# Performance work log

Measured on AMD Instinct MI355X. Metric: run time of the kernel, lower is better.

## Reference

```python
import jax, jax.numpy as jnp
import numpy as np

N_NODES = 50000


def _add_self_loops(edge_index, n):
    loop = jnp.arange(n, dtype=edge_index.dtype)
    src = jnp.concatenate([edge_index[0], loop])
    dst = jnp.concatenate([edge_index[1], loop])
    return src, dst


def _gcn_norm(src, dst, n):
    # symmetric normalization with unit edge weights (edge_weight=None)
    w = jnp.ones(src.shape[0], dtype=jnp.float32)
    deg = jax.ops.segment_sum(w, dst, num_segments=n)  # [N]
    dinv = jnp.where(deg > 0, jax.lax.rsqrt(jnp.maximum(deg, 1.0)), 0.0)
    return dinv[src] * w * dinv[dst]  # [E+N]


def _gcn_conv(x, src, dst, norm, W, b, n):
    h = x @ W                                   # [N, out] transform first (PyG order)
    msg = h[src] * norm[:, None]                # [E+N, out] gather + scale
    agg = jax.ops.segment_sum(msg, dst, num_segments=n)  # scatter-add
    return agg + b


def setup_inputs() -> dict:
    key = jax.random.key(0)
    k1, k2, k3, k4 = jax.random.split(key, 4)
    N, E, IN, HID, OUT = N_NODES, 1600000, 512, 64, 7
    x = jax.random.normal(k1, (N, IN), dtype=jnp.float32)
    edge_index = jax.random.randint(k2, (2, E), 0, N, dtype=jnp.int64)
    W1 = jax.random.normal(k3, (IN, HID), dtype=jnp.float32) * (1.0 / np.sqrt(IN))
    b1 = jnp.zeros((HID,), dtype=jnp.float32)
    W2 = jax.random.normal(k4, (HID, OUT), dtype=jnp.float32) * (1.0 / np.sqrt(HID))
    b2 = jnp.zeros((OUT,), dtype=jnp.float32)
    return {"x": x, "edge_index": edge_index, "W1": W1, "b1": b1, "W2": W2, "b2": b2}


def reference(x, edge_index, W1, b1, W2, b2):
    n = x.shape[0]
    src, dst = _add_self_loops(edge_index, n)
    norm = _gcn_norm(src, dst, n)  # graph-only, shared across layers
    h = _gcn_conv(x, src, dst, norm, W1, b1, n)
    h = jax.nn.relu(h)
    # dropout is identity in eval/inference mode
    out = _gcn_conv(h, src, dst, norm, W2, b2, n)
    return out
```

## Files before the change

### kernel.cpp

```cpp
#include <hip/hip_runtime.h>

#define N_NODES 50000
#define N_EDGES 1600000
#define DIM_IN  512
#define DIM_HID 64
#define DIM_OUT 7
#define NBUCK   196
#define PART_BLOCKS 256

using u16 = unsigned short;
using bf16x8 = __attribute__((ext_vector_type(8))) __bf16;
using f32x4  = __attribute__((ext_vector_type(4))) float;

__device__ __forceinline__ float bf2f(u16 u) {
    union { float f; unsigned int i; } v;
    v.i = ((unsigned int)u) << 16;
    return v.f;
}

__device__ __forceinline__ u16 f2bf(float f) {
    union { float f; unsigned int i; } v;
    v.f = f;
    unsigned int r = 0x7FFFu + ((v.i >> 16) & 1u);
    return (u16)((v.i + r) >> 16);
}

__device__ __forceinline__ float bflo(unsigned int u) {
    union { float f; unsigned int i; } v;
    v.i = u << 16;
    return v.f;
}

__device__ __forceinline__ float bfhi(unsigned int u) {
    union { float f; unsigned int i; } v;
    v.i = u & 0xFFFF0000u;
    return v.f;
}

__global__ void k_detect(const u16* __restrict__ xw, const int* __restrict__ ei32,
                         int* __restrict__ flags) {
    __shared__ int s1[256];
    __shared__ int s2[256];
    int t = threadIdx.x;
    u16 w = xw[2 * t];
    int e = (w >> 7) & 0xFF;
    s1[t] = (e >= 100 && e <= 140) ? 1 : 0;
    s2[t] = (ei32[2 * t + 1] != 0) ? 1 : 0;
    __syncthreads();
    for (int off = 128; off >= 1; off >>= 1) {
        if (t < off) { s1[t] += s1[t + off]; s2[t] += s2[t + off]; }
        __syncthreads();
    }
    if (t == 0) {
        flags[0] = (s1[0] >= 200) ? 0 : 1;
        flags[1] = (s2[0] == 0) ? 1 : 0;
    }
}

__device__ __forceinline__ int ld_edge(const int* ei, int i64f, size_t idx) {
    if (i64f) return ei[2 * idx];
    return ei[idx];
}

__global__ void k_count(const int* __restrict__ ei, const int* __restrict__ flags,
                        int* __restrict__ gbsum, int* __restrict__ cnt) {
    __shared__ int hist[NBUCK];
    int t = threadIdx.x;
    int i64f = flags[1];
    const int CH = (N_EDGES + PART_BLOCKS - 1) / PART_BLOCKS;
    int lo = blockIdx.x * CH;
    int hi = lo + CH; if (hi > N_EDGES) hi = N_EDGES;
    if (t < NBUCK) hist[t] = 0;
    __syncthreads();
    for (int i = lo + t; i < hi; i += 1024) {
        int s = ld_edge(ei, i64f, (size_t)i);
        int d = ld_edge(ei, i64f, (size_t)N_EDGES + i);
        if ((unsigned)d < (unsigned)N_NODES && (unsigned)s < (unsigned)N_NODES)
            atomicAdd(&hist[d >> 8], 1);
    }
    __syncthreads();
    if (t < NBUCK) {
        int h = hist[t];
        cnt[t * PART_BLOCKS + blockIdx.x] = h;
        if (h > 0) atomicAdd(&gbsum[t], h);
    }
}

__global__ void k_pb(const int* __restrict__ gbsum, int* __restrict__ cnt,
                     int* __restrict__ bbase, int* __restrict__ rowptr) {
    __shared__ int g0[256];
    __shared__ int gs[256];
    __shared__ int sc[256];
    int b = blockIdx.x, t = threadIdx.x;
    int gv = (t < NBUCK) ? gbsum[t] : 0;
    g0[t] = gv;
    gs[t] = gv;
    __syncthreads();
    for (int off = 1; off < 256; off <<= 1) {
        int u = (t >= off) ? gs[t - off] : 0;
        __syncthreads();
        gs[t] += u;
        __syncthreads();
    }
    int bb = gs[b] - g0[b];
    if (t == 0) bbase[b] = bb;
    if (b == 0 && t == 255) rowptr[N_NODES] = gs[255];
    int v = cnt[b * PART_BLOCKS + t];
    sc[t] = v;
    __syncthreads();
    for (int off = 1; off < 256; off <<= 1) {
        int u = (t >= off) ? sc[t - off] : 0;
        __syncthreads();
        sc[t] += u;
        __syncthreads();
    }
    cnt[b * PART_BLOCKS + t] = bb + sc[t] - v;
}

__global__ void k_part(const int* __restrict__ ei, const int* __restrict__ flags,
                       const int* __restrict__ cnt, unsigned int* __restrict__ ebuf) {
    __shared__ int cur[NBUCK];
    int t = threadIdx.x, blk = blockIdx.x;
    int i64f = flags[1];
    const int CH = (N_EDGES + PART_BLOCKS - 1) / PART_BLOCKS;
    int lo = blk * CH;
    int hi = lo + CH; if (hi > N_EDGES) hi = N_EDGES;
    if (t < NBUCK) cur[t] = cnt[t * PART_BLOCKS + blk];
    __syncthreads();
    for (int i = lo + t; i < hi; i += 1024) {
        int s = ld_edge(ei, i64f, (size_t)i);
        int d = ld_edge(ei, i64f, (size_t)N_EDGES + i);
        if ((unsigned)d < (unsigned)N_NODES && (unsigned)s < (unsigned)N_NODES) {
            int pos = atomicAdd(&cur[d >> 8], 1);
            if ((unsigned)pos < (unsigned)N_EDGES)
                ebuf[pos] = ((unsigned)s << 8) | (unsigned)(d & 255);
        }
    }
}

__global__ void k_cfill(const unsigned int* __restrict__ ebuf,
                        const int* __restrict__ bbase, const int* __restrict__ gbsum,
                        int* __restrict__ rowptr, float* __restrict__ dinv,
                        int* __restrict__ col) {
    __shared__ int dcnt[256];
    __shared__ int sc[256];
    __shared__ int cur[256];
    int b = blockIdx.x, t = threadIdx.x;
    int e0 = bbase[b];
    int e1 = e0 + gbsum[b];
    if (t < 256) dcnt[t] = 0;
    __syncthreads();
    for (int e = e0 + t; e < e1; e += 1024)
        atomicAdd(&dcnt[ebuf[e] & 255u], 1);
    __syncthreads();
    int v = 0;
    if (t < 256) { v = dcnt[t]; sc[t] = v; }
    __syncthreads();
    for (int off = 1; off < 256; off <<= 1) {
        int u = (t >= off && t < 256) ? sc[t - off] : 0;
        __syncthreads();
        if (t < 256) sc[t] += u;
        __syncthreads();
    }
    if (t < 256) {
        int row0 = e0 + sc[t] - v;
        cur[t] = row0;
        int idx = b * 256 + t;
        if (idx < N_NODES) {
            rowptr[idx] = row0;
            dinv[idx] = rsqrtf((float)(v + 1));
        }
    }
    __syncthreads();
    for (int e = e0 + t; e < e1; e += 1024) {
        unsigned int x = ebuf[e];
        int p = atomicAdd(&cur[x & 255u], 1);
        if ((unsigned)p < (unsigned)N_EDGES) col[p] = (int)(x >> 8);
    }
}

__global__ void k_tw1(const void* __restrict__ W1, const int* __restrict__ flags,
                      u16* __restrict__ W1T) {
    int i = blockIdx.x * blockDim.x + threadIdx.x;
    if (i < DIM_IN * DIM_HID) {
        int n = i >> 9;
        int k = i & 511;
        if (flags[0]) W1T[i] = f2bf(((const float*)W1)[k * DIM_HID + n]);
        else          W1T[i] = ((const u16*)W1)[k * DIM_HID + n];
    }
}

__launch_bounds__(256)
__global__ void k_gemm1(const void* __restrict__ xraw, const u16* __restrict__ W1T,
                        const int* __restrict__ flags, const float* __restrict__ dinv,
                        u16* __restrict__ hs) {
    int f32f = flags[0];
    int wave = threadIdx.x >> 6;
    int lane = threadIdx.x & 63;
    int m16 = lane & 15;
    int quad = lane >> 4;
    int rbase = blockIdx.x * 64 + wave * 16;
    int ra = rbase + m16;
    if (ra > N_NODES - 1) ra = N_NODES - 1;
    const u16*   xrow_b = (const u16*)xraw   + (size_t)ra * DIM_IN + quad * 8;
    const float* xrow_f = (const float*)xraw + (size_t)ra * DIM_IN + quad * 8;
    const u16* wrow = W1T + (size_t)m16 * DIM_IN + quad * 8;

    f32x4 acc0 = {0.f, 0.f, 0.f, 0.f};
    f32x4 acc1 = {0.f, 0.f, 0.f, 0.f};
    f32x4 acc2 = {0.f, 0.f, 0.f, 0.f};
    f32x4 acc3 = {0.f, 0.f, 0.f, 0.f};

    for (int ks = 0; ks < DIM_IN / 32; ++ks) {
        bf16x8 a;
        if (f32f) {
            const float4* q = reinterpret_cast<const float4*>(xrow_f + ks * 32);
            float4 p0 = q[0], p1 = q[1];
            union { bf16x8 v; u16 s[8]; } u;
            u.s[0] = f2bf(p0.x); u.s[1] = f2bf(p0.y); u.s[2] = f2bf(p0.z); u.s[3] = f2bf(p0.w);
            u.s[4] = f2bf(p1.x); u.s[5] = f2bf(p1.y); u.s[6] = f2bf(p1.z); u.s[7] = f2bf(p1.w);
            a = u.v;
        } else {
            a = *reinterpret_cast<const bf16x8*>(xrow_b + ks * 32);
        }
        bf16x8 b0 = *reinterpret_cast<const bf16x8*>(wrow + ks * 32);
        bf16x8 b1 = *reinterpret_cast<const bf16x8*>(wrow + ks * 32 + 16 * DIM_IN);
        bf16x8 b2 = *reinterpret_cast<const bf16x8*>(wrow + ks * 32 + 32 * DIM_IN);
        bf16x8 b3 = *reinterpret_cast<const bf16x8*>(wrow + ks * 32 + 48 * DIM_IN);
        acc0 = __builtin_amdgcn_mfma_f32_16x16x32_bf16(a, b0, acc0, 0, 0, 0);
        acc1 = __builtin_amdgcn_mfma_f32_16x16x32_bf16(a, b1, acc1, 0, 0, 0);
        acc2 = __builtin_amdgcn_mfma_f32_16x16x32_bf16(a, b2, acc2, 0, 0, 0);
        acc3 = __builtin_amdgcn_mfma_f32_16x16x32_bf16(a, b3, acc3, 0, 0, 0);
    }

#pragma unroll
    for (int i = 0; i < 4; ++i) {
        int r = rbase + quad * 4 + i;
        if (r < N_NODES) {
            float dv = dinv[r];
            u16* orow = hs + (size_t)r * DIM_HID;
            orow[ 0 + m16] = f2bf(acc0[i] * dv);
            orow[16 + m16] = f2bf(acc1[i] * dv);
            orow[32 + m16] = f2bf(acc2[i] * dv);
            orow[48 + m16] = f2bf(acc3[i] * dv);
        }
    }
}

__launch_bounds__(256)
__global__ void k_agg1(const u16* __restrict__ hs, const int* __restrict__ rowptr,
                       const int* __restrict__ col, const float* __restrict__ dinv,
                       const void* __restrict__ b1, const void* __restrict__ W2,
                       const int* __restrict__ flags, float* __restrict__ zs) {
    __shared__ float xh[4][64];
    int f32f = flags[0];
    int wave = threadIdx.x >> 6;
    int lane = threadIdx.x & 63;
    int g = lane >> 3;
    int q = lane & 7;
    int d = blockIdx.x * 4 + wave;
    int start = rowptr[d], end = rowptr[d + 1];
    if (start < 0) start = 0;
    if (end > N_EDGES) end = N_EDGES;
    if (end < start) end = start;

    float a[8];
#pragma unroll
    for (int k = 0; k < 8; ++k) a[k] = 0.f;

    const uint4* hs4 = reinterpret_cast<const uint4*>(hs);
    const int* cp = col + start;
    int ne = end - start;
    int nfull = ne >> 3;

    int it = 0;
    for (; it + 4 <= nfull; it += 4) {
        int c0 = cp[(it + 0) * 8 + g];
        int c1 = cp[(it + 1) * 8 + g];
        int c2 = cp[(it + 2) * 8 + g];
        int c3 = cp[(it + 3) * 8 + g];
        uint4 r0 = hs4[(size_t)c0 * 8 + q];
        uint4 r1 = hs4[(size_t)c1 * 8 + q];
        uint4 r2 = hs4[(size_t)c2 * 8 + q];
        uint4 r3 = hs4[(size_t)c3 * 8 + q];
#pragma unroll
        for (int u = 0; u < 4; ++u) {
            uint4 r = (u == 0) ? r0 : (u == 1) ? r1 : (u == 2) ? r2 : r3;
            a[0] += bflo(r.x); a[1] += bfhi(r.x);
            a[2] += bflo(r.y); a[3] += bfhi(r.y);
            a[4] += bflo(r.z); a[5] += bfhi(r.z);
            a[6] += bflo(r.w); a[7] += bfhi(r.w);
        }
    }
    for (; it < nfull; ++it) {
        int c = cp[it * 8 + g];
        uint4 r = hs4[(size_t)c * 8 + q];
        a[0] += bflo(r.x); a[1] += bfhi(r.x);
        a[2] += bflo(r.y); a[3] += bfhi(r.y);
        a[4] += bflo(r.z); a[5] += bfhi(r.z);
        a[6] += bflo(r.w); a[7] += bfhi(r.w);
    }
    {
        int e = start + nfull * 8 + g;
        if (e < end) {
            int c = col[e];
            uint4 r = hs4[(size_t)c * 8 + q];
            a[0] += bflo(r.x); a[1] += bfhi(r.x);
            a[2] += bflo(r.y); a[3] += bfhi(r.y);
            a[4] += bflo(r.z); a[5] += bfhi(r.z);
            a[6] += bflo(r.w); a[7] += bfhi(r.w);
        }
    }

#pragma unroll
    for (int k = 0; k < 8; ++k) {
        a[k] += __shfl_xor(a[k], 8);
        a[k] += __shfl_xor(a[k], 16);
        a[k] += __shfl_xor(a[k], 32);
    }

    {
        uint4 r = hs4[(size_t)d * 8 + q];
        a[0] += bflo(r.x); a[1] += bfhi(r.x);
        a[2] += bflo(r.y); a[3] += bfhi(r.y);
        a[4] += bflo(r.z); a[5] += bfhi(r.z);
        a[6] += bflo(r.w); a[7] += bfhi(r.w);
    }

    float dv = dinv[d];
    float h[8];
    if (f32f) {
        const float* bf = (const float*)b1 + q * 8;
#pragma unroll
        for (int k = 0; k < 8; ++k) h[k] = fmaxf(a[k] * dv + bf[k], 0.f);
    } else {
        const u16* bb = (const u16*)b1 + q * 8;
#pragma unroll
        for (int k = 0; k < 8; ++k) h[k] = fmaxf(a[k] * dv + bf2f(bb[k]), 0.f);
    }

    if (g == 0) {
#pragma unroll
        for (int k = 0; k < 8; ++k) xh[wave][q * 8 + k] = h[k];
    }
    __syncthreads();
    float h2 = xh[wave][lane];

    float p[7];
#pragma unroll
    for (int f = 0; f < 7; ++f) {
        float w = f32f ? ((const float*)W2)[lane * DIM_OUT + f]
                       : bf2f(((const u16*)W2)[lane * DIM_OUT + f]);
        p[f] = h2 * w;
    }
#pragma unroll
    for (int off = 32; off >= 1; off >>= 1) {
#pragma unroll
        for (int f = 0; f < 7; ++f) p[f] += __shfl_xor(p[f], off);
    }
    if (lane == 0) {
#pragma unroll
        for (int f = 0; f < 7; ++f) zs[(size_t)d * 8 + f] = p[f] * dv;
        zs[(size_t)d * 8 + 7] = 0.f;
    }
}

__launch_bounds__(256)
__global__ void k_agg2(const float* __restrict__ zs, const int* __restrict__ rowptr,
                       const int* __restrict__ col, const float* __restrict__ dinv,
                       const void* __restrict__ b2, const int* __restrict__ flags,
                       float* __restrict__ out) {
    int f32f = flags[0];
    int wave = threadIdx.x >> 6;
    int lane = threadIdx.x & 63;
    int d = blockIdx.x * 4 + wave;
    if (d >= N_NODES) return;
    int f = lane & 7;
    int g = lane >> 3;
    int start = rowptr[d], end = rowptr[d + 1];
    if (start < 0) start = 0;
    if (end > N_EDGES) end = N_EDGES;
    if (end < start) end = start;

    float acc = 0.f;
    for (int e = start + g; e < end; e += 8)
        acc += zs[(size_t)col[e] * 8 + f];

    acc += __shfl_xor(acc, 8);
    acc += __shfl_xor(acc, 16);
    acc += __shfl_xor(acc, 32);

    if (lane < 7) {
        float b2v = f32f ? ((const float*)b2)[lane] : bf2f(((const u16*)b2)[lane]);
        float tot = (acc + zs[(size_t)d * 8 + lane]) * dinv[d] + b2v;
        out[(size_t)d * DIM_OUT + lane] = tot;
    }
}

extern "C" void kernel_launch(void* const* d_in, const int* in_sizes, int n_in,
                              void* d_out, int out_size, void* d_ws, size_t ws_size,
                              hipStream_t stream) {
    const void* x  = d_in[0];
    const int*  ei = (const int*)d_in[1];
    const void* W1 = d_in[2];
    const void* b1 = d_in[3];
    const void* W2 = d_in[4];
    const void* b2 = d_in[5];

    char* ws = (char*)d_ws;
    size_t off = 0;
    auto alloc = [&](size_t bytes) -> void* {
        void* p = ws + off;
        off = (off + bytes + 255) & ~(size_t)255;
        return p;
    };
    int*   flags  = (int*)alloc(32);
    int*   rowptr = (int*)alloc((size_t)(N_NODES + 1) * 4);
    int*   gbsum  = (int*)alloc((size_t)NBUCK * 4);
    int*   bbase  = (int*)alloc((size_t)NBUCK * 4);
    int*   cnt    = (int*)alloc((size_t)NBUCK * PART_BLOCKS * 4);
    float* dinv   = (float*)alloc((size_t)N_NODES * 4);
    u16*   W1T    = (u16*)alloc((size_t)DIM_IN * DIM_HID * 2);
    unsigned int* ebuf = (unsigned int*)alloc((size_t)N_EDGES * 4);
    int*   colb   = (int*)alloc((size_t)N_EDGES * 4);
    u16*   hs     = (u16*)alloc((size_t)N_NODES * DIM_HID * 2);
    float* zs     = (float*)alloc((size_t)N_NODES * 8 * 4);
    float* out    = (float*)d_out;

    hipMemsetAsync(gbsum, 0, (size_t)NBUCK * 4, stream);
    k_detect<<<1, 256, 0, stream>>>((const u16*)x, ei, flags);
    k_count<<<PART_BLOCKS, 1024, 0, stream>>>(ei, flags, gbsum, cnt);
    k_pb   <<<NBUCK, 256, 0, stream>>>(gbsum, cnt, bbase, rowptr);
    k_part <<<PART_BLOCKS, 1024, 0, stream>>>(ei, flags, cnt, ebuf);
    k_cfill<<<NBUCK, 1024, 0, stream>>>(ebuf, bbase, gbsum, rowptr, dinv, colb);
    k_tw1  <<<(DIM_IN * DIM_HID + 255) / 256, 256, 0, stream>>>(W1, flags, W1T);
    k_gemm1<<<(N_NODES + 63) / 64, 256, 0, stream>>>(x, W1T, flags, dinv, hs);
    k_agg1 <<<(N_NODES + 3) / 4, 256, 0, stream>>>(hs, rowptr, colb, dinv, b1, W2, flags, zs);
    k_agg2 <<<(N_NODES + 3) / 4, 256, 0, stream>>>(zs, rowptr, colb, dinv, b2, flags, out);
}
```

Measured before the change: 296.1 us.

## Fuse CSR build into fixed-capacity bucket scatter and merge prep kernels

Replaces the count / prefix-sum / partition kernel sequence with a single scatter kernel. Each block reserves space in a fixed-capacity per-bucket buffer through a global atomic, and the bucket prefix sum moves into the column-fill kernel. Detection, counter zeroing and the W1 transpose are merged into one single-block prep kernel, which removes the memset and several launches. The cost is a larger edge buffer and silent truncation of any bucket holding more than BCAP edges. It also makes the W1 transpose serial on one block and the intra-bucket edge order nondeterministic.

```diff
diff --git a/kernel.cpp b/kernel.cpp
--- a/kernel.cpp
+++ b/kernel.cpp
@@ -7,6 +7,7 @@
 #define DIM_OUT 7
 #define NBUCK   196
 #define PART_BLOCKS 256
+#define BCAP    16384
 
 using u16 = unsigned short;
 using bf16x8 = __attribute__((ext_vector_type(8))) __bf16;
@@ -37,121 +38,114 @@
     return v.f;
 }
 
-__global__ void k_detect(const u16* __restrict__ xw, const int* __restrict__ ei32,
-                         int* __restrict__ flags) {
+__device__ __forceinline__ int ld_edge(const int* ei, int i64f, size_t idx) {
+    if (i64f) return ei[2 * idx];
+    return ei[idx];
+}
+
+__launch_bounds__(1024)
+__global__ void k_prep(const u16* __restrict__ xw, const int* __restrict__ ei32,
+                       const void* __restrict__ W1, int* __restrict__ flags,
+                       int* __restrict__ gcnt, u16* __restrict__ W1T) {
     __shared__ int s1[256];
     __shared__ int s2[256];
+    __shared__ int fl0;
     int t = threadIdx.x;
-    u16 w = xw[2 * t];
-    int e = (w >> 7) & 0xFF;
-    s1[t] = (e >= 100 && e <= 140) ? 1 : 0;
-    s2[t] = (ei32[2 * t + 1] != 0) ? 1 : 0;
+    if (t < 256) {
+        u16 w = xw[2 * t];
+        int e = (w >> 7) & 0xFF;
+        s1[t] = (e >= 100 && e <= 140) ? 1 : 0;
+        s2[t] = (ei32[2 * t + 1] != 0) ? 1 : 0;
+    }
     __syncthreads();
     for (int off = 128; off >= 1; off >>= 1) {
         if (t < off) { s1[t] += s1[t + off]; s2[t] += s2[t + off]; }
         __syncthreads();
     }
     if (t == 0) {
-        flags[0] = (s1[0] >= 200) ? 0 : 1;
+        int f0 = (s1[0] >= 200) ? 0 : 1;
+        flags[0] = f0;
         flags[1] = (s2[0] == 0) ? 1 : 0;
-    }
-}
-
-__device__ __forceinline__ int ld_edge(const int* ei, int i64f, size_t idx) {
-    if (i64f) return ei[2 * idx];
-    return ei[idx];
-}
-
-__global__ void k_count(const int* __restrict__ ei, const int* __restrict__ flags,
-                        int* __restrict__ gbsum, int* __restrict__ cnt) {
+        fl0 = f0;
+    }
+    if (t < NBUCK) gcnt[t] = 0;
+    __syncthreads();
+    int f32f = fl0;
+    for (int i = t; i < DIM_IN * DIM_HID; i += 1024) {
+        int n = i >> 9;
+        int k = i & 511;
+        if (f32f) W1T[i] = f2bf(((const float*)W1)[k * DIM_HID + n]);
+        else      W1T[i] = ((const u16*)W1)[k * DIM_HID + n];
+    }
+}
+
+__launch_bounds__(1024)
+__global__ void k_scat(const int* __restrict__ ei, const int* __restrict__ flags,
+                       int* __restrict__ gcnt, unsigned int* __restrict__ ebuf) {
     __shared__ int hist[NBUCK];
-    int t = threadIdx.x;
-    int i64f = flags[1];
-    const int CH = (N_EDGES + PART_BLOCKS - 1) / PART_BLOCKS;
-    int lo = blockIdx.x * CH;
-    int hi = lo + CH; if (hi > N_EDGES) hi = N_EDGES;
-    if (t < NBUCK) hist[t] = 0;
-    __syncthreads();
-    for (int i = lo + t; i < hi; i += 1024) {
-        int s = ld_edge(ei, i64f, (size_t)i);
-        int d = ld_edge(ei, i64f, (size_t)N_EDGES + i);
-        if ((unsigned)d < (unsigned)N_NODES && (unsigned)s < (unsigned)N_NODES)
-            atomicAdd(&hist[d >> 8], 1);
-    }
-    __syncthreads();
-    if (t < NBUCK) {
-        int h = hist[t];
-        cnt[t * PART_BLOCKS + blockIdx.x] = h;
-        if (h > 0) atomicAdd(&gbsum[t], h);
-    }
-}
-
-__global__ void k_pb(const int* __restrict__ gbsum, int* __restrict__ cnt,
-                     int* __restrict__ bbase, int* __restrict__ rowptr) {
-    __shared__ int g0[256];
-    __shared__ int gs[256];
-    __shared__ int sc[256];
-    int b = blockIdx.x, t = threadIdx.x;
-    int gv = (t < NBUCK) ? gbsum[t] : 0;
-    g0[t] = gv;
-    gs[t] = gv;
-    __syncthreads();
-    for (int off = 1; off < 256; off <<= 1) {
-        int u = (t >= off) ? gs[t - off] : 0;
-        __syncthreads();
-        gs[t] += u;
-        __syncthreads();
-    }
-    int bb = gs[b] - g0[b];
-    if (t == 0) bbase[b] = bb;
-    if (b == 0 && t == 255) rowptr[N_NODES] = gs[255];
-    int v = cnt[b * PART_BLOCKS + t];
-    sc[t] = v;
-    __syncthreads();
-    for (int off = 1; off < 256; off <<= 1) {
-        int u = (t >= off) ? sc[t - off] : 0;
-        __syncthreads();
-        sc[t] += u;
-        __syncthreads();
-    }
-    cnt[b * PART_BLOCKS + t] = bb + sc[t] - v;
-}
-
-__global__ void k_part(const int* __restrict__ ei, const int* __restrict__ flags,
-                       const int* __restrict__ cnt, unsigned int* __restrict__ ebuf) {
     __shared__ int cur[NBUCK];
     int t = threadIdx.x, blk = blockIdx.x;
     int i64f = flags[1];
     const int CH = (N_EDGES + PART_BLOCKS - 1) / PART_BLOCKS;
     int lo = blk * CH;
     int hi = lo + CH; if (hi > N_EDGES) hi = N_EDGES;
-    if (t < NBUCK) cur[t] = cnt[t * PART_BLOCKS + blk];
+    if (t < NBUCK) hist[t] = 0;
+    __syncthreads();
+    for (int i = lo + t; i < hi; i += 1024) {
+        int s = ld_edge(ei, i64f, (size_t)i);
+        int d = ld_edge(ei, i64f, (size_t)N_EDGES + i);
+        if ((unsigned)d < (unsigned)N_NODES && (unsigned)s < (unsigned)N_NODES)
+            atomicAdd(&hist[d >> 8], 1);
+    }
+    __syncthreads();
+    if (t < NBUCK) {
+        int h = hist[t];
+        cur[t] = (h > 0) ? atomicAdd(&gcnt[t], h) : 0;
+    }
     __syncthreads();
     for (int i = lo + t; i < hi; i += 1024) {
         int s = ld_edge(ei, i64f, (size_t)i);
         int d = ld_edge(ei, i64f, (size_t)N_EDGES + i);
         if ((unsigned)d < (unsigned)N_NODES && (unsigned)s < (unsigned)N_NODES) {
-            int pos = atomicAdd(&cur[d >> 8], 1);
-            if ((unsigned)pos < (unsigned)N_EDGES)
-                ebuf[pos] = ((unsigned)s << 8) | (unsigned)(d & 255);
-        }
-    }
-}
-
+            int b = d >> 8;
+            int off = atomicAdd(&cur[b], 1);
+            if ((unsigned)off < (unsigned)BCAP)
+                ebuf[(size_t)b * BCAP + off] = ((unsigned)s << 8) | (unsigned)(d & 255);
+        }
+    }
+}
+
+__launch_bounds__(1024)
 __global__ void k_cfill(const unsigned int* __restrict__ ebuf,
-                        const int* __restrict__ bbase, const int* __restrict__ gbsum,
+                        const int* __restrict__ gcnt,
                         int* __restrict__ rowptr, float* __restrict__ dinv,
                         int* __restrict__ col) {
+    __shared__ int gs[256];
     __shared__ int dcnt[256];
     __shared__ int sc[256];
     __shared__ int cur[256];
     int b = blockIdx.x, t = threadIdx.x;
-    int e0 = bbase[b];
-    int e1 = e0 + gbsum[b];
+    if (t < 256) {
+        int gv = (t < NBUCK) ? gcnt[t] : 0;
+        if (gv > BCAP) gv = BCAP;
+        gs[t] = gv;
+    }
+    __syncthreads();
+    for (int off = 1; off < 256; off <<= 1) {
+        int u = (t >= off && t < 256) ? gs[t - off] : 0;
+        __syncthreads();
+        if (t < 256) gs[t] += u;
+        __syncthreads();
+    }
+    int cntb = gcnt[b]; if (cntb > BCAP) cntb = BCAP;
+    int cb = gs[b] - cntb;
+    if (b == 0 && t == 0) rowptr[N_NODES] = gs[255];
+    const unsigned int* eb = ebuf + (size_t)b * BCAP;
+
     if (t < 256) dcnt[t] = 0;
     __syncthreads();
-    for (int e = e0 + t; e < e1; e += 1024)
-        atomicAdd(&dcnt[ebuf[e] & 255u], 1);
+    for (int e = t; e < cntb; e += 1024)
+        atomicAdd(&dcnt[eb[e] & 255u], 1);
     __syncthreads();
     int v = 0;
     if (t < 256) { v = dcnt[t]; sc[t] = v; }
@@ -163,7 +157,7 @@
         __syncthreads();
     }
     if (t < 256) {
-        int row0 = e0 + sc[t] - v;
+        int row0 = cb + sc[t] - v;
         cur[t] = row0;
         int idx = b * 256 + t;
         if (idx < N_NODES) {
@@ -172,21 +166,10 @@
         }
     }
     __syncthreads();
-    for (int e = e0 + t; e < e1; e += 1024) {
-        unsigned int x = ebuf[e];
+    for (int e = t; e < cntb; e += 1024) {
+        unsigned int x = eb[e];
         int p = atomicAdd(&cur[x & 255u], 1);
         if ((unsigned)p < (unsigned)N_EDGES) col[p] = (int)(x >> 8);
-    }
-}
-
-__global__ void k_tw1(const void* __restrict__ W1, const int* __restrict__ flags,
-                      u16* __restrict__ W1T) {
-    int i = blockIdx.x * blockDim.x + threadIdx.x;
-    if (i < DIM_IN * DIM_HID) {
-        int n = i >> 9;
-        int k = i & 511;
-        if (flags[0]) W1T[i] = f2bf(((const float*)W1)[k * DIM_HID + n]);
-        else          W1T[i] = ((const u16*)W1)[k * DIM_HID + n];
     }
 }
 
@@ -416,24 +399,18 @@
     };
     int*   flags  = (int*)alloc(32);
     int*   rowptr = (int*)alloc((size_t)(N_NODES + 1) * 4);
-    int*   gbsum  = (int*)alloc((size_t)NBUCK * 4);
-    int*   bbase  = (int*)alloc((size_t)NBUCK * 4);
-    int*   cnt    = (int*)alloc((size_t)NBUCK * PART_BLOCKS * 4);
+    int*   gcnt   = (int*)alloc((size_t)NBUCK * 4);
     float* dinv   = (float*)alloc((size_t)N_NODES * 4);
     u16*   W1T    = (u16*)alloc((size_t)DIM_IN * DIM_HID * 2);
-    unsigned int* ebuf = (unsigned int*)alloc((size_t)N_EDGES * 4);
+    unsigned int* ebuf = (unsigned int*)alloc((size_t)NBUCK * BCAP * 4);
     int*   colb   = (int*)alloc((size_t)N_EDGES * 4);
     u16*   hs     = (u16*)alloc((size_t)N_NODES * DIM_HID * 2);
     float* zs     = (float*)alloc((size_t)N_NODES * 8 * 4);
     float* out    = (float*)d_out;
 
-    hipMemsetAsync(gbsum, 0, (size_t)NBUCK * 4, stream);
-    k_detect<<<1, 256, 0, stream>>>((const u16*)x, ei, flags);
-    k_count<<<PART_BLOCKS, 1024, 0, stream>>>(ei, flags, gbsum, cnt);
-    k_pb   <<<NBUCK, 256, 0, stream>>>(gbsum, cnt, bbase, rowptr);
-    k_part <<<PART_BLOCKS, 1024, 0, stream>>>(ei, flags, cnt, ebuf);
-    k_cfill<<<NBUCK, 1024, 0, stream>>>(ebuf, bbase, gbsum, rowptr, dinv, colb);
-    k_tw1  <<<(DIM_IN * DIM_HID + 255) / 256, 256, 0, stream>>>(W1, flags, W1T);
+    k_prep <<<1, 1024, 0, stream>>>((const u16*)x, ei, W1, flags, gcnt, W1T);
+    k_scat <<<PART_BLOCKS, 1024, 0, stream>>>(ei, flags, gcnt, ebuf);
+    k_cfill<<<NBUCK, 1024, 0, stream>>>(ebuf, gcnt, rowptr, dinv, colb);
     k_gemm1<<<(N_NODES + 63) / 64, 256, 0, stream>>>(x, W1T, flags, dinv, hs);
     k_agg1 <<<(N_NODES + 3) / 4, 256, 0, stream>>>(hs, rowptr, colb, dinv, b1, W2, flags, zs);
     k_agg2 <<<(N_NODES + 3) / 4, 256, 0, stream>>>(zs, rowptr, colb, dinv, b2, flags, out);
```

New measurement: 309.1 us. 1.04x slower.
